# Performance work log

Hardware: AMD Instinct MI355X
Metric: run time of the kernel (lower is better)

The kernel has to match this reference:

```python
import jax, jax.numpy as jnp
import numpy as np

B, S, D = 8, 1024, 128
EPS = 1e-7
LN_EPS = 1e-3  # keras LayerNormalization default


def setup_inputs() -> dict:
    key = jax.random.key(0)
    ks = jax.random.split(key, 8)
    sd = 1.0 / np.sqrt(D)
    return {
        "x": jax.random.normal(ks[0], (B, S, D), jnp.float32),
        "Wq": jax.random.normal(ks[1], (D, D), jnp.float32) * sd,
        "bq": jnp.zeros((D,), jnp.float32),
        "Wm": jax.random.normal(ks[2], (D, D), jnp.float32) * sd,
        "bm": jnp.zeros((D,), jnp.float32),
        "Ww": jax.random.normal(ks[3], (D, 1), jnp.float32) * sd,
        "bw": jnp.zeros((1,), jnp.float32),
        "Wc": jax.random.normal(ks[4], (D, 1), jnp.float32) * sd,
        "bc": jnp.zeros((1,), jnp.float32),
        "emb_map": jax.random.normal(ks[5], (D, D, D), jnp.float32) * 0.02,
        "gamma": jnp.ones((D,), jnp.float32),
        "beta": jnp.zeros((D,), jnp.float32),
    }


def reference(x, Wq, bq, Wm, bm, Ww, bw, Wc, bc, emb_map, gamma, beta):
    b_, s_, d_ = x.shape
    q = x @ Wq + bq                      # [B,S,D]
    m = jax.nn.sigmoid(x @ Wm + bm)      # [B,S,D]
    w = jax.nn.relu(x @ Ww + bw)         # [B,S,1]
    c = jax.nn.relu(x @ Wc + bc)         # [B,S,1]

    # distances: for query pos i, preceding pos j (j<i) has distance i-j
    idx = jnp.arange(s_)
    dist = (idx[:, None] - idx[None, :]).astype(x.dtype)   # [S,S]
    valid = dist > 0                                       # strict causal
    # cosh positional decay, zero outside causal window -> [B,S,S]
    pe = jnp.where(valid[None], 1.0 / jnp.cosh((dist[None] - c) / (w + EPS)), 0.0)

    # angle between (pe * x_j * m_i + eps) and (q_i + eps), expanded analytically
    qp = q + EPS
    t1 = jnp.einsum('bjd,bid->bij', x, m * qp)             # sum_d x_j m_i q'_i
    s1 = jnp.einsum('bjd,bid->bij', x, m)                  # sum_d x_j m_i
    s2 = jnp.einsum('bjd,bid->bij', x * x, m * m)          # sum_d (x_j m_i)^2
    dot = pe * t1 + EPS * jnp.sum(qp, axis=-1)[:, :, None]
    na = jnp.sqrt(pe * pe * s2 + 2.0 * EPS * pe * s1 + d_ * EPS * EPS)
    nb = jnp.linalg.norm(qp, axis=-1)[:, :, None]
    cos = jnp.where(valid[None], dot / (na * nb), 0.0)
    angle = jnp.where(valid[None], jnp.arccos(cos), 0.0)   # [B,S,S]

    # query_result_i = sum_j pe*angle * x_j  -> [B,S,D]
    qr = jnp.einsum('bij,bjd->bid', pe * angle, x)

    # embedding matrix: current_token (rows) outer query_result (cols),
    # contracted against rank-3 map: out[b,s,d] = sum_{j,k} x[b,s,j] qr[b,s,k] map[d,j,k]
    em = jnp.einsum('bsj,bsk->bsjk', x, qr).reshape(b_, s_, d_ * d_)
    mapped = em @ emb_map.reshape(d_, d_ * d_).T           # [B,S,D]

    res = mapped + x
    mu = jnp.mean(res, axis=-1, keepdims=True)
    var = jnp.var(res, axis=-1, keepdims=True)
    out = (res - mu) / jnp.sqrt(var + LN_EPS) * gamma + beta
    return out  # dropout is identity at inference
```

## Files before the change

### kernel.cpp

```cpp
#include <hip/hip_runtime.h>
#include <hip/hip_bf16.h>
#include <math.h>

#define DD 128
#define SS 1024
#define NROWS 8192
#define EPSF 1e-7f
#define LN_EPSF 1e-3f
#define TCUT 30.0f

typedef __attribute__((ext_vector_type(8))) short bf16x8;
typedef __attribute__((ext_vector_type(8))) _Float16 f16x8;
typedef __attribute__((ext_vector_type(4))) float f32x4;
typedef __attribute__((ext_vector_type(16))) float f32x16;

__device__ __forceinline__ void gload_lds16(const void* g, void* l) {
    __builtin_amdgcn_global_load_lds(
        (const __attribute__((address_space(1))) unsigned int*)g,
        (__attribute__((address_space(3))) unsigned int*)l, 16, 0, 0);
}
__device__ __forceinline__ short f2bf(float v) {
    union { __hip_bfloat16 h; short s; } u;
    u.h = __float2bfloat16(v);
    return u.s;
}
__device__ __forceinline__ float bf2f(short s) {
    union { __hip_bfloat16 h; short s; } u; u.s = s;
    return __bfloat162float(u.h);
}
__device__ __forceinline__ short f2h(float v) {
    union { _Float16 h; short s; } u;
    u.h = (_Float16)v;
    return u.s;
}
__device__ __forceinline__ unsigned int pkmul_f16(unsigned int a, unsigned int b) {
    unsigned int r;
    asm("v_pk_mul_f16 %0, %1, %2" : "=v"(r) : "v"(a), "v"(b));
    return r;
}
__device__ __forceinline__ unsigned int f2h_dup(float v) {
    union { _Float16 h[2]; unsigned int u; } c;
    c.h[0] = (_Float16)v; c.h[1] = c.h[0];
    return c.u;
}

__global__ __launch_bounds__(256) void k0a_emb(const float* __restrict__ emb,
                                               short* __restrict__ embB) {
    __shared__ float lt[128][132];
    int j = blockIdx.x, t = threadIdx.x;
    {
        int d = t >> 1, kh = (t & 1) * 64;
        const float* src = emb + (size_t)d * 16384 + (size_t)j * 128 + kh;
#pragma unroll
        for (int q = 0; q < 16; ++q)
            *(float4*)&lt[d][kh + q * 4] = *(const float4*)(src + q * 4);
    }
    __syncthreads();
#pragma unroll
    for (int i = 0; i < 8; ++i) {
        int idx = i * 256 + t;
        int l = idx & 63, s = (idx >> 6) & 7, dt = (idx >> 9) & 3;
        const float* p = &lt[dt * 32 + (l & 31)][s * 16 + (l >> 5) * 8];
        union { bf16x8 v; short sa[8]; } ob;
#pragma unroll
        for (int e = 0; e < 8; ++e) ob.sa[e] = f2h(p[e]);
        *(bf16x8*)(embB + (size_t)j * 16384 + dt * 4096 + s * 512 + (size_t)l * 8) = ob.v;
    }
}

__global__ __launch_bounds__(256) void k0w_split(const float* __restrict__ Wq,
        const float* __restrict__ Wm, short* __restrict__ Wfrag) {
    int T = blockIdx.x * 256 + threadIdx.x;
    int e = T & 7, l = (T >> 3) & 63, ks = (T >> 9) & 3, nt = (T >> 11) & 7,
        mat = (T >> 14) & 1;
    int k = ks * 32 + ((l >> 4) & 3) * 8 + e;
    int c = nt * 16 + (l & 15);
    float v = (mat ? Wm : Wq)[k * 128 + c];
    short h = f2bf(v);
    float lo = v - bf2f(h);
    Wfrag[((((size_t)(mat * 2 + 0) * 8 + nt) * 4 + ks) * 64 + l) * 8 + e] = h;
    Wfrag[((((size_t)(mat * 2 + 1) * 8 + nt) * 4 + ks) * 64 + l) * 8 + e] = f2bf(lo);
}

__global__ __launch_bounds__(256) void k0c_xsplit(const float* __restrict__ x,
        const float* __restrict__ Ww, const float* __restrict__ bw,
        const float* __restrict__ Wc, const float* __restrict__ bc,
        short* __restrict__ xh2, short* __restrict__ xl2,
        float* __restrict__ scal) {
    __shared__ float xs[32][129];
    int rb = blockIdx.x, t = threadIdx.x;
    {
        int r = t >> 3, d0 = (t & 7) * 16;
        const float4* src = (const float4*)(x + (size_t)(rb * 32 + r) * 128 + d0);
#pragma unroll
        for (int q = 0; q < 4; ++q) *(float4*)&xs[r][d0 + q * 4] = src[q];
    }
    __syncthreads();
    int ks = (t >> 5) & 3, rf = t >> 7, l0 = (t & 31) * 2;
    union { bf16x8 v[2]; short s[16]; } hb, lb;
#pragma unroll
    for (int li = 0; li < 2; ++li) {
        int l = l0 + li;
        const float* p = &xs[rf * 16 + (l & 15)][ks * 32 + ((l >> 4) & 3) * 8];
#pragma unroll
        for (int e = 0; e < 8; ++e) {
            float v = p[e];
            short h = f2bf(v);
            hb.s[li * 8 + e] = h;
            lb.s[li * 8 + e] = f2bf(v - bf2f(h));
        }
    }
    {
        short* d1 = xh2 + (size_t)rb * 4096 + (size_t)t * 16;
        short* d2 = xl2 + (size_t)rb * 4096 + (size_t)t * 16;
        *(bf16x8*)d1 = hb.v[0]; *(bf16x8*)(d1 + 8) = hb.v[1];
        *(bf16x8*)d2 = lb.v[0]; *(bf16x8*)(d2 + 8) = lb.v[1];
    }
    int rr = t >> 3, seg = t & 7;
    float pw = 0.f, pc = 0.f;
#pragma unroll
    for (int dq = 0; dq < 16; ++dq) {
        float xv = xs[rr][seg * 16 + dq];
        pw = fmaf(xv, Ww[seg * 16 + dq], pw);
        pc = fmaf(xv, Wc[seg * 16 + dq], pc);
    }
    pw += __shfl_xor(pw, 1); pw += __shfl_xor(pw, 2); pw += __shfl_xor(pw, 4);
    pc += __shfl_xor(pc, 1); pc += __shfl_xor(pc, 2); pc += __shfl_xor(pc, 4);
    if (seg == 0) {
        scal[(size_t)(rb * 32 + rr) * 4 + 0] = fmaxf(pw + bw[0], 0.f);
        scal[(size_t)(rb * 32 + rr) * 4 + 1] = fmaxf(pc + bc[0], 0.f);
    }
}

__global__ __launch_bounds__(256) void k1_mfma(
    const short* __restrict__ xh2, const short* __restrict__ xl2,
    const short* __restrict__ Wfrag,
    const float* __restrict__ bq, const float* __restrict__ bm,
    float* __restrict__ mq, float* __restrict__ mo, float* __restrict__ scal)
{
    __shared__ __align__(16) short wl[65536];
    __shared__ float red[32][4][2];
    int t = threadIdx.x, w = t >> 6, l = t & 63;
    int l15 = l & 15, g = l >> 4;
    int row0 = blockIdx.x * 32;
#pragma unroll
    for (int it = 0; it < 32; ++it)
        gload_lds16(Wfrag + (size_t)(it * 256 + t) * 8, wl + (size_t)(it * 256 + w * 64) * 8);
    const short* xb  = xh2 + (size_t)blockIdx.x * 4096;
    const short* xlb = xl2 + (size_t)blockIdx.x * 4096;
    bf16x8 Ah[2][4], Al[2][4];
#pragma unroll
    for (int rf = 0; rf < 2; ++rf)
#pragma unroll
        for (int ks = 0; ks < 4; ++ks) {
            size_t o = ((size_t)(rf * 4 + ks) * 64 + l) * 8;
            Ah[rf][ks] = *(const bf16x8*)(xb + o);
            Al[rf][ks] = *(const bf16x8*)(xlb + o);
        }
    __syncthreads();
    f32x4 accq[2][2] = {}, accm[2][2] = {};
#pragma unroll
    for (int ntp = 0; ntp < 2; ++ntp) {
        int nt = w * 2 + ntp;
#pragma unroll
        for (int ks = 0; ks < 4; ++ks) {
            bf16x8 bhq = *(const bf16x8*)(wl + ((size_t)(0  + nt) * 4 + ks) * 512 + l * 8);
            bf16x8 blq = *(const bf16x8*)(wl + ((size_t)(8  + nt) * 4 + ks) * 512 + l * 8);
            bf16x8 bhm = *(const bf16x8*)(wl + ((size_t)(16 + nt) * 4 + ks) * 512 + l * 8);
            bf16x8 blm = *(const bf16x8*)(wl + ((size_t)(24 + nt) * 4 + ks) * 512 + l * 8);
#pragma unroll
            for (int rf = 0; rf < 2; ++rf) {
                accq[rf][ntp] = __builtin_amdgcn_mfma_f32_16x16x32_bf16(Ah[rf][ks], bhq, accq[rf][ntp], 0, 0, 0);
                accq[rf][ntp] = __builtin_amdgcn_mfma_f32_16x16x32_bf16(Ah[rf][ks], blq, accq[rf][ntp], 0, 0, 0);
                accq[rf][ntp] = __builtin_amdgcn_mfma_f32_16x16x32_bf16(Al[rf][ks], bhq, accq[rf][ntp], 0, 0, 0);
                accm[rf][ntp] = __builtin_amdgcn_mfma_f32_16x16x32_bf16(Ah[rf][ks], bhm, accm[rf][ntp], 0, 0, 0);
                accm[rf][ntp] = __builtin_amdgcn_mfma_f32_16x16x32_bf16(Ah[rf][ks], blm, accm[rf][ntp], 0, 0, 0);
                accm[rf][ntp] = __builtin_amdgcn_mfma_f32_16x16x32_bf16(Al[rf][ks], bhm, accm[rf][ntp], 0, 0, 0);
            }
        }
    }
    float sq1[2][4] = {{0,0,0,0},{0,0,0,0}};
    float sq2[2][4] = {{0,0,0,0},{0,0,0,0}};
#pragma unroll
    for (int ntp = 0; ntp < 2; ++ntp) {
        int c = (w * 2 + ntp) * 16 + l15;
        float bqv = bq[c] + EPSF, bmv = bm[c];
#pragma unroll
        for (int rf = 0; rf < 2; ++rf)
#pragma unroll
            for (int reg = 0; reg < 4; ++reg) {
                int rloc = rf * 16 + g * 4 + reg;
                float qp = accq[rf][ntp][reg] + bqv;
                float mv = 1.0f / (1.0f + expf(-(accm[rf][ntp][reg] + bmv)));
                size_t o = (size_t)(row0 + rloc) * 128 + c;
                mq[o] = mv * qp;
                mo[o] = mv;
                sq1[rf][reg] += qp;
                sq2[rf][reg] += qp * qp;
            }
    }
#pragma unroll
    for (int rf = 0; rf < 2; ++rf)
#pragma unroll
        for (int reg = 0; reg < 4; ++reg) {
            float a = sq1[rf][reg], b = sq2[rf][reg];
            a += __shfl_xor(a, 1); a += __shfl_xor(a, 2);
            a += __shfl_xor(a, 4); a += __shfl_xor(a, 8);
            b += __shfl_xor(b, 1); b += __shfl_xor(b, 2);
            b += __shfl_xor(b, 4); b += __shfl_xor(b, 8);
            if (l15 == 0) {
                red[rf * 16 + g * 4 + reg][w][0] = a;
                red[rf * 16 + g * 4 + reg][w][1] = b;
            }
        }
    __syncthreads();
    if (t < 32) {
        float a = red[t][0][0] + red[t][1][0] + red[t][2][0] + red[t][3][0];
        float b = red[t][0][1] + red[t][1][1] + red[t][2][1] + red[t][3][1];
        scal[(size_t)(row0 + t) * 4 + 2] = a;
        scal[(size_t)(row0 + t) * 4 + 3] = sqrtf(b);
    }
}

__global__ __launch_bounds__(256) void k2_qr(
    const float* __restrict__ x,
    const float* __restrict__ mq, const float* __restrict__ mo,
    const float* __restrict__ scal, short* __restrict__ qrh2)
{
    int row = blockIdx.x;
    int i = row & (SS - 1);
    const float* xb = x + (size_t)(row - i) * DD;
    int t = threadIdx.x, w = t >> 6, l = t & 63;
    int sub = l >> 4, q = l & 15;
    int qo = q * 8;

    float mqv[8], mov[8];
    {
        const float* mp = mq + (size_t)row * DD + qo;
        float4 a = *(const float4*)mp, b = *(const float4*)(mp + 4);
        mqv[0] = a.x; mqv[1] = a.y; mqv[2] = a.z; mqv[3] = a.w;
        mqv[4] = b.x; mqv[5] = b.y; mqv[6] = b.z; mqv[7] = b.w;
        const float* op = mo + (size_t)row * DD + qo;
        float4 c = *(const float4*)op, d = *(const float4*)(op + 4);
        mov[0] = c.x; mov[1] = c.y; mov[2] = c.z; mov[3] = c.w;
        mov[4] = d.x; mov[5] = d.y; mov[6] = d.z; mov[7] = d.w;
    }
    float wv = scal[row * 4 + 0], cv = scal[row * 4 + 1];
    float sumqp = scal[row * 4 + 2], nb = scal[row * 4 + 3];
    float wi = wv + EPSF;
    float dmaxf = cv + TCUT * wi;
    int dmax = (dmaxf >= (float)i) ? i : (int)dmaxf;

    float acc[8] = {0.f, 0.f, 0.f, 0.f, 0.f, 0.f, 0.f, 0.f};
    int nit = (dmax + 15) >> 4;
    int dbase = 1 + w * 4 + sub;
    for (int it = 0; it < nit; ++it) {
        int dist = dbase + it * 16;
        float xv[8];
        if (dist <= dmax) {
            const float* xp = xb + (size_t)(i - dist) * DD + qo;
            float4 a = *(const float4*)xp, b = *(const float4*)(xp + 4);
            xv[0] = a.x; xv[1] = a.y; xv[2] = a.z; xv[3] = a.w;
            xv[4] = b.x; xv[5] = b.y; xv[6] = b.z; xv[7] = b.w;
        } else {
#pragma unroll
            for (int e = 0; e < 8; ++e) xv[e] = 0.f;
        }
        float t1 = 0.f, s1 = 0.f, s2 = 0.f;
#pragma unroll
        for (int e = 0; e < 8; ++e) {
            float xm = xv[e] * mov[e];
            t1 = fmaf(xv[e], mqv[e], t1);
            s1 += xm;
            s2 = fmaf(xm, xm, s2);
        }
#pragma unroll
        for (int off = 1; off < 16; off <<= 1) {
            t1 += __shfl_xor(t1, off);
            s1 += __shfl_xor(s1, off);
            s2 += __shfl_xor(s2, off);
        }
        float tt = ((float)dist - cv) / wi;
        float pe = 1.0f / coshf(tt);
        float dotv = fmaf(pe, t1, EPSF * sumqp);
        float na = sqrtf(fmaf(pe * pe, s2,
                         fmaf(2.0f * EPSF * pe, s1, (float)DD * EPSF * EPSF)));
        float cosv = fminf(1.0f, fmaxf(-1.0f, dotv / (na * nb)));
        float ang = acosf(cosv);
        float wgt = pe * ang;
#pragma unroll
        for (int e = 0; e < 8; ++e) acc[e] = fmaf(wgt, xv[e], acc[e]);
    }
#pragma unroll
    for (int e = 0; e < 8; ++e) {
        acc[e] += __shfl_xor(acc[e], 16);
        acc[e] += __shfl_xor(acc[e], 32);
    }
    __shared__ float sq[4][DD];
    if (l < 16) {
#pragma unroll
        for (int e = 0; e < 8; ++e) sq[w][qo + e] = acc[e];
    }
    __syncthreads();
    if (t < DD) {
        float v = sq[0][t] + sq[1][t] + sq[2][t] + sq[3][t];
        int rbq = row >> 7, rr = row & 127, rt2 = rr >> 5, lp = rr & 31;
        int k = t;
        qrh2[(((size_t)(rbq * 4 + rt2) * 8 + (k >> 4)) * 64
              + (lp + 32 * ((k >> 3) & 1))) * 8 + (k & 7)] = f2h(v);
    }
}

__global__ __launch_bounds__(256, 2) void k3_gemm(
    const float* __restrict__ x, const short* __restrict__ embB,
    const short* __restrict__ qrh2, float* __restrict__ part)
{
    __shared__ unsigned int xtd[32][66];
    __shared__ float sof[64][128];
    int t = threadIdx.x, w = t >> 6, l = t & 63;
    int l31 = l & 31, hi = l >> 5;
    int dh = w & 1, sh = w >> 1;
    int rb = blockIdx.x, js = blockIdx.y;

    {
        int r = t >> 2, q = t & 3;
        const float* xp = x + (size_t)(rb * 64 + r) * 128 + js * 32 + q * 8;
        float4 a = *(const float4*)xp, b = *(const float4*)(xp + 4);
        xtd[q * 8 + 0][r] = f2h_dup(a.x); xtd[q * 8 + 1][r] = f2h_dup(a.y);
        xtd[q * 8 + 2][r] = f2h_dup(a.z); xtd[q * 8 + 3][r] = f2h_dup(a.w);
        xtd[q * 8 + 4][r] = f2h_dup(b.x); xtd[q * 8 + 5][r] = f2h_dup(b.y);
        xtd[q * 8 + 6][r] = f2h_dup(b.z); xtd[q * 8 + 7][r] = f2h_dup(b.w);
    }

    unsigned int qrp[2][4][4];
#pragma unroll
    for (int rt = 0; rt < 2; ++rt) {
        int R32 = rb * 2 + rt;
#pragma unroll
        for (int s = 0; s < 4; ++s) {
            union { f16x8 v; unsigned int u[4]; } qb;
            qb.v = *(const f16x8*)(qrh2
                + (((size_t)R32 * 8 + sh * 4 + s) * 64 + l) * 8);
#pragma unroll
            for (int p = 0; p < 4; ++p) qrp[rt][s][p] = qb.u[p];
        }
    }

    const short* Bbase = embB + (size_t)(js * 32) * 16384
                         + (size_t)(dh * 2) * 4096 + (size_t)(sh * 4) * 512
                         + (size_t)l * 8;

    f32x16 acc[2][2];
#pragma unroll
    for (int rt = 0; rt < 2; ++rt)
#pragma unroll
        for (int i = 0; i < 2; ++i)
#pragma unroll
            for (int q = 0; q < 16; ++q) acc[rt][i][q] = 0.f;

#define LOADB(BN, JJ)                                                       \
    {                                                                       \
        const short* bp_ = Bbase + (size_t)(JJ) * 16384;                    \
        _Pragma("unroll")                                                   \
        for (int i = 0; i < 2; ++i)                                         \
            _Pragma("unroll")                                               \
            for (int s = 0; s < 4; ++s)                                     \
                BN[i][s] = *(const f16x8*)(bp_ + i * 4096 + s * 512);       \
    }

#define COMPUTE(BN, JJ)                                                     \
    {                                                                       \
        unsigned int xs0 = xtd[JJ][l31], xs1 = xtd[JJ][32 + l31];           \
        _Pragma("unroll")                                                   \
        for (int s = 0; s < 4; ++s) {                                       \
            union { f16x8 v; unsigned int u[4]; } a0, a1;                   \
            _Pragma("unroll")                                               \
            for (int p = 0; p < 4; ++p) {                                   \
                a0.u[p] = pkmul_f16(qrp[0][s][p], xs0);                     \
                a1.u[p] = pkmul_f16(qrp[1][s][p], xs1);                     \
            }                                                               \
            acc[0][0] = __builtin_amdgcn_mfma_f32_32x32x16_f16(             \
                a0.v, BN[0][s], acc[0][0], 0, 0, 0);                        \
            acc[0][1] = __builtin_amdgcn_mfma_f32_32x32x16_f16(             \
                a0.v, BN[1][s], acc[0][1], 0, 0, 0);                        \
            acc[1][0] = __builtin_amdgcn_mfma_f32_32x32x16_f16(             \
                a1.v, BN[0][s], acc[1][0], 0, 0, 0);                        \
            acc[1][1] = __builtin_amdgcn_mfma_f32_32x32x16_f16(             \
                a1.v, BN[1][s], acc[1][1], 0, 0, 0);                        \
        }                                                                   \
    }

    f16x8 B0[2][4], B1[2][4];
    LOADB(B0, 0)
    __syncthreads();

#pragma unroll 1
    for (int jj = 0; jj < 32; jj += 2) {
        if (jj + 1 < 32) LOADB(B1, jj + 1)
        COMPUTE(B0, jj)
        if (jj + 2 < 32) LOADB(B0, jj + 2)
        COMPUTE(B1, jj + 1)
    }
#undef LOADB
#undef COMPUTE

    __syncthreads();
    if (sh == 0) {
#pragma unroll
        for (int rt = 0; rt < 2; ++rt)
#pragma unroll
            for (int i = 0; i < 2; ++i)
#pragma unroll
                for (int q = 0; q < 16; ++q) {
                    int r = rt * 32 + (q & 3) + 8 * (q >> 2) + 4 * hi;
                    sof[r][(dh * 2 + i) * 32 + l31] = acc[rt][i][q];
                }
    }
    __syncthreads();
    if (sh == 1) {
#pragma unroll
        for (int rt = 0; rt < 2; ++rt)
#pragma unroll
            for (int i = 0; i < 2; ++i)
#pragma unroll
                for (int q = 0; q < 16; ++q) {
                    int r = rt * 32 + (q & 3) + 8 * (q >> 2) + 4 * hi;
                    sof[r][(dh * 2 + i) * 32 + l31] += acc[rt][i][q];
                }
    }
    __syncthreads();
#pragma unroll
    for (int i = 0; i < 8; ++i) {
        int idx = i * 256 + t;
        int r = idx >> 5, c4 = (idx & 31) * 4;
        float4 v = *(const float4*)&sof[r][c4];
        *(float4*)(part + (size_t)js * (NROWS * DD)
                   + (size_t)(rb * 64 + r) * 128 + c4) = v;
    }
}

__global__ __launch_bounds__(256) void k4_ln(
    const float* __restrict__ x, const float* __restrict__ part,
    const float* __restrict__ gamma, const float* __restrict__ beta,
    float* __restrict__ out)
{
    int wave = threadIdx.x >> 6, lane = threadIdx.x & 63;
    int row = blockIdx.x * 4 + wave;
    size_t base = (size_t)row * DD;
    float r0 = x[base + lane], r1 = x[base + lane + 64];
#pragma unroll
    for (int p = 0; p < 4; ++p) {
        r0 += part[(size_t)p * NROWS * DD + base + lane];
        r1 += part[(size_t)p * NROWS * DD + base + lane + 64];
    }
    float s = r0 + r1, s2 = r0 * r0 + r1 * r1;
#pragma unroll
    for (int off = 32; off > 0; off >>= 1) {
        s += __shfl_xor(s, off);
        s2 += __shfl_xor(s2, off);
    }
    float mu = s * (1.0f / DD);
    float var = s2 * (1.0f / DD) - mu * mu;
    var = fmaxf(var, 0.0f);
    float rs = rsqrtf(var + LN_EPSF);
    out[base + lane] = (r0 - mu) * rs * gamma[lane] + beta[lane];
    out[base + lane + 64] = (r1 - mu) * rs * gamma[lane + 64] + beta[lane + 64];
}

extern "C" void kernel_launch(void* const* d_in, const int* in_sizes, int n_in,
                              void* d_out, int out_size, void* d_ws, size_t ws_size,
                              hipStream_t stream) {
    const float* x     = (const float*)d_in[0];
    const float* Wq    = (const float*)d_in[1];
    const float* bq    = (const float*)d_in[2];
    const float* Wm    = (const float*)d_in[3];
    const float* bm    = (const float*)d_in[4];
    const float* Ww    = (const float*)d_in[5];
    const float* bw    = (const float*)d_in[6];
    const float* Wc    = (const float*)d_in[7];
    const float* bc    = (const float*)d_in[8];
    const float* emb   = (const float*)d_in[9];
    const float* gamma = (const float*)d_in[10];
    const float* beta  = (const float*)d_in[11];
    float* out = (float*)d_out;
    float* ws  = (float*)d_ws;

    short* embB  = (short*)ws;
    short* qrh2  = (short*)(ws + 1048576);
    float* scal  = ws + 1572864;
    float* part  = ws + 1605632;
    float* tr    = ws + 1605632;
    short* xh2   = (short*)tr;
    short* xl2   = (short*)(tr + 524288);
    float* mq    = tr + 1048576;
    float* mo    = tr + 2097152;
    short* Wfrag = (short*)(tr + 3145728);

    hipLaunchKernelGGL(k0a_emb,   dim3(128),    dim3(256), 0, stream, emb, embB);
    hipLaunchKernelGGL(k0w_split, dim3(256),    dim3(256), 0, stream, Wq, Wm, Wfrag);
    hipLaunchKernelGGL(k0c_xsplit,dim3(256),    dim3(256), 0, stream,
                       x, Ww, bw, Wc, bc, xh2, xl2, scal);
    hipLaunchKernelGGL(k1_mfma,   dim3(256),    dim3(256), 0, stream,
                       xh2, xl2, Wfrag, bq, bm, mq, mo, scal);
    hipLaunchKernelGGL(k2_qr,     dim3(8192),   dim3(256), 0, stream,
                       x, mq, mo, scal, qrh2);
    hipLaunchKernelGGL(k3_gemm,   dim3(128, 4), dim3(256), 0, stream,
                       x, embB, qrh2, part);
    hipLaunchKernelGGL(k4_ln,     dim3(2048),   dim3(256), 0, stream,
                       x, part, gamma, beta, out);
}
```

Baseline: 90.84 us.

## Retile embedding GEMM with LDS double-buffered B and bf16 partial sums

```diff
diff --git a/kernel.cpp b/kernel.cpp
--- a/kernel.cpp
+++ b/kernel.cpp
@@ -42,6 +42,11 @@
     union { _Float16 h[2]; unsigned int u; } c;
     c.h[0] = (_Float16)v; c.h[1] = c.h[0];
     return c.u;
+}
+__device__ __forceinline__ unsigned int pack_bf16(float lo, float hi) {
+    unsigned int r;
+    asm("v_cvt_pk_bf16_f32 %0, %1, %2" : "=v"(r) : "v"(lo), "v"(hi));
+    return r;
 }
 
 __global__ __launch_bounds__(256) void k0a_emb(const float* __restrict__ emb,
@@ -313,43 +318,46 @@
 
 __global__ __launch_bounds__(256, 2) void k3_gemm(
     const float* __restrict__ x, const short* __restrict__ embB,
-    const short* __restrict__ qrh2, float* __restrict__ part)
+    const short* __restrict__ qrh2, short* __restrict__ partb)
 {
-    __shared__ unsigned int xtd[32][66];
-    __shared__ float sof[64][128];
+    __shared__ __align__(16) short bB[2][16384];
+    __shared__ unsigned int xtd[16][132];
     int t = threadIdx.x, w = t >> 6, l = t & 63;
     int l31 = l & 31, hi = l >> 5;
-    int dh = w & 1, sh = w >> 1;
+    int rh = w >> 1, dh = w & 1;
     int rb = blockIdx.x, js = blockIdx.y;
 
     {
-        int r = t >> 2, q = t & 3;
-        const float* xp = x + (size_t)(rb * 64 + r) * 128 + js * 32 + q * 8;
+        int r = t >> 1, jq = (t & 1) * 8;
+        const float* xp = x + (size_t)(rb * 128 + r) * 128 + js * 16 + jq;
         float4 a = *(const float4*)xp, b = *(const float4*)(xp + 4);
-        xtd[q * 8 + 0][r] = f2h_dup(a.x); xtd[q * 8 + 1][r] = f2h_dup(a.y);
-        xtd[q * 8 + 2][r] = f2h_dup(a.z); xtd[q * 8 + 3][r] = f2h_dup(a.w);
-        xtd[q * 8 + 4][r] = f2h_dup(b.x); xtd[q * 8 + 5][r] = f2h_dup(b.y);
-        xtd[q * 8 + 6][r] = f2h_dup(b.z); xtd[q * 8 + 7][r] = f2h_dup(b.w);
-    }
-
-    unsigned int qrp[2][4][4];
+        xtd[jq + 0][r] = f2h_dup(a.x); xtd[jq + 1][r] = f2h_dup(a.y);
+        xtd[jq + 2][r] = f2h_dup(a.z); xtd[jq + 3][r] = f2h_dup(a.w);
+        xtd[jq + 4][r] = f2h_dup(b.x); xtd[jq + 5][r] = f2h_dup(b.y);
+        xtd[jq + 6][r] = f2h_dup(b.z); xtd[jq + 7][r] = f2h_dup(b.w);
+    }
+
+    {
+        const short* src = embB + (size_t)(js * 16) * 16384;
+#pragma unroll
+        for (int i = 0; i < 8; ++i)
+            gload_lds16(src + (size_t)(i * 256 + t) * 8,
+                        &bB[0][0] + (size_t)(i * 256 + w * 64) * 8);
+    }
+
+    unsigned int qrp[2][8][4];
 #pragma unroll
     for (int rt = 0; rt < 2; ++rt) {
-        int R32 = rb * 2 + rt;
-#pragma unroll
-        for (int s = 0; s < 4; ++s) {
+        int R32 = rb * 4 + rh * 2 + rt;
+#pragma unroll
+        for (int s = 0; s < 8; ++s) {
             union { f16x8 v; unsigned int u[4]; } qb;
-            qb.v = *(const f16x8*)(qrh2
-                + (((size_t)R32 * 8 + sh * 4 + s) * 64 + l) * 8);
+            qb.v = *(const f16x8*)(qrh2 + (((size_t)R32 * 8 + s) * 64 + l) * 8);
 #pragma unroll
             for (int p = 0; p < 4; ++p) qrp[rt][s][p] = qb.u[p];
         }
     }
 
-    const short* Bbase = embB + (size_t)(js * 32) * 16384
-                         + (size_t)(dh * 2) * 4096 + (size_t)(sh * 4) * 512
-                         + (size_t)l * 8;
-
     f32x16 acc[2][2];
 #pragma unroll
     for (int rt = 0; rt < 2; ++rt)
@@ -358,89 +366,63 @@
 #pragma unroll
             for (int q = 0; q < 16; ++q) acc[rt][i][q] = 0.f;
 
-#define LOADB(BN, JJ)                                                       \
-    {                                                                       \
-        const short* bp_ = Bbase + (size_t)(JJ) * 16384;                    \
-        _Pragma("unroll")                                                   \
-        for (int i = 0; i < 2; ++i)                                         \
-            _Pragma("unroll")                                               \
-            for (int s = 0; s < 4; ++s)                                     \
-                BN[i][s] = *(const f16x8*)(bp_ + i * 4096 + s * 512);       \
-    }
-
-#define COMPUTE(BN, JJ)                                                     \
-    {                                                                       \
-        unsigned int xs0 = xtd[JJ][l31], xs1 = xtd[JJ][32 + l31];           \
-        _Pragma("unroll")                                                   \
-        for (int s = 0; s < 4; ++s) {                                       \
-            union { f16x8 v; unsigned int u[4]; } a0, a1;                   \
-            _Pragma("unroll")                                               \
-            for (int p = 0; p < 4; ++p) {                                   \
-                a0.u[p] = pkmul_f16(qrp[0][s][p], xs0);                     \
-                a1.u[p] = pkmul_f16(qrp[1][s][p], xs1);                     \
-            }                                                               \
-            acc[0][0] = __builtin_amdgcn_mfma_f32_32x32x16_f16(             \
-                a0.v, BN[0][s], acc[0][0], 0, 0, 0);                        \
-            acc[0][1] = __builtin_amdgcn_mfma_f32_32x32x16_f16(             \
-                a0.v, BN[1][s], acc[0][1], 0, 0, 0);                        \
-            acc[1][0] = __builtin_amdgcn_mfma_f32_32x32x16_f16(             \
-                a1.v, BN[0][s], acc[1][0], 0, 0, 0);                        \
-            acc[1][1] = __builtin_amdgcn_mfma_f32_32x32x16_f16(             \
-                a1.v, BN[1][s], acc[1][1], 0, 0, 0);                        \
-        }                                                                   \
-    }
-
-    f16x8 B0[2][4], B1[2][4];
-    LOADB(B0, 0)
     __syncthreads();
 
 #pragma unroll 1
-    for (int jj = 0; jj < 32; jj += 2) {
-        if (jj + 1 < 32) LOADB(B1, jj + 1)
-        COMPUTE(B0, jj)
-        if (jj + 2 < 32) LOADB(B0, jj + 2)
-        COMPUTE(B1, jj + 1)
-    }
-#undef LOADB
-#undef COMPUTE
-
-    __syncthreads();
-    if (sh == 0) {
-#pragma unroll
-        for (int rt = 0; rt < 2; ++rt)
-#pragma unroll
-            for (int i = 0; i < 2; ++i)
-#pragma unroll
-                for (int q = 0; q < 16; ++q) {
-                    int r = rt * 32 + (q & 3) + 8 * (q >> 2) + 4 * hi;
-                    sof[r][(dh * 2 + i) * 32 + l31] = acc[rt][i][q];
-                }
-    }
-    __syncthreads();
-    if (sh == 1) {
-#pragma unroll
-        for (int rt = 0; rt < 2; ++rt)
-#pragma unroll
-            for (int i = 0; i < 2; ++i)
-#pragma unroll
-                for (int q = 0; q < 16; ++q) {
-                    int r = rt * 32 + (q & 3) + 8 * (q >> 2) + 4 * hi;
-                    sof[r][(dh * 2 + i) * 32 + l31] += acc[rt][i][q];
-                }
-    }
-    __syncthreads();
+    for (int jj = 0; jj < 16; ++jj) {
+        int cur = jj & 1;
+        if (jj < 15) {
+            const short* src = embB + (size_t)(js * 16 + jj + 1) * 16384;
+#pragma unroll
+            for (int i = 0; i < 8; ++i)
+                gload_lds16(src + (size_t)(i * 256 + t) * 8,
+                            &bB[cur ^ 1][0] + (size_t)(i * 256 + w * 64) * 8);
+        }
+        unsigned int xs0 = xtd[jj][rh * 64 + l31];
+        unsigned int xs1 = xtd[jj][rh * 64 + 32 + l31];
+        const short* bb = &bB[cur][0] + (size_t)(dh * 2) * 4096 + (size_t)l * 8;
+#pragma unroll
+        for (int s = 0; s < 8; ++s) {
+            f16x8 Bd0 = *(const f16x8*)(bb + s * 512);
+            f16x8 Bd1 = *(const f16x8*)(bb + 4096 + s * 512);
+            union { f16x8 v; unsigned int u[4]; } a0, a1;
+#pragma unroll
+            for (int p = 0; p < 4; ++p) {
+                a0.u[p] = pkmul_f16(qrp[0][s][p], xs0);
+                a1.u[p] = pkmul_f16(qrp[1][s][p], xs1);
+            }
+            acc[0][0] = __builtin_amdgcn_mfma_f32_32x32x16_f16(a0.v, Bd0, acc[0][0], 0, 0, 0);
+            acc[0][1] = __builtin_amdgcn_mfma_f32_32x32x16_f16(a0.v, Bd1, acc[0][1], 0, 0, 0);
+            acc[1][0] = __builtin_amdgcn_mfma_f32_32x32x16_f16(a1.v, Bd0, acc[1][0], 0, 0, 0);
+            acc[1][1] = __builtin_amdgcn_mfma_f32_32x32x16_f16(a1.v, Bd1, acc[1][1], 0, 0, 0);
+        }
+        __syncthreads();
+    }
+
+    short* sofh = &bB[0][0];
+#pragma unroll
+    for (int rt = 0; rt < 2; ++rt)
+#pragma unroll
+        for (int i = 0; i < 2; ++i)
+#pragma unroll
+            for (int q = 0; q < 16; ++q) {
+                int r = rh * 64 + rt * 32 + (q & 3) + 8 * (q >> 2) + 4 * hi;
+                int c = dh * 64 + i * 32 + l31;
+                sofh[r * 136 + c] = f2h(0.f), sofh[r * 136 + c] = f2bf(acc[rt][i][q]);
+            }
+    __syncthreads();
+    size_t pbase = (size_t)js * ((size_t)NROWS * DD);
 #pragma unroll
     for (int i = 0; i < 8; ++i) {
         int idx = i * 256 + t;
-        int r = idx >> 5, c4 = (idx & 31) * 4;
-        float4 v = *(const float4*)&sof[r][c4];
-        *(float4*)(part + (size_t)js * (NROWS * DD)
-                   + (size_t)(rb * 64 + r) * 128 + c4) = v;
+        int r = idx >> 4, c8 = (idx & 15) * 8;
+        *(bf16x8*)(partb + pbase + (size_t)(rb * 128 + r) * 128 + c8)
+            = *(const bf16x8*)(sofh + r * 136 + c8);
     }
 }
 
 __global__ __launch_bounds__(256) void k4_ln(
-    const float* __restrict__ x, const float* __restrict__ part,
+    const float* __restrict__ x, const short* __restrict__ partb,
     const float* __restrict__ gamma, const float* __restrict__ beta,
     float* __restrict__ out)
 {
@@ -449,9 +431,9 @@
     size_t base = (size_t)row * DD;
     float r0 = x[base + lane], r1 = x[base + lane + 64];
 #pragma unroll
-    for (int p = 0; p < 4; ++p) {
-        r0 += part[(size_t)p * NROWS * DD + base + lane];
-        r1 += part[(size_t)p * NROWS * DD + base + lane + 64];
+    for (int p = 0; p < 8; ++p) {
+        r0 += bf2f(partb[(size_t)p * 1048576 + base + lane]);
+        r1 += bf2f(partb[(size_t)p * 1048576 + base + lane + 64]);
     }
     float s = r0 + r1, s2 = r0 * r0 + r1 * r1;
 #pragma unroll
@@ -488,7 +470,7 @@
     short* embB  = (short*)ws;
     short* qrh2  = (short*)(ws + 1048576);
     float* scal  = ws + 1572864;
-    float* part  = ws + 1605632;
+    short* partb = (short*)(ws + 1605632);
     float* tr    = ws + 1605632;
     short* xh2   = (short*)tr;
     short* xl2   = (short*)(tr + 524288);
@@ -504,8 +486,8 @@
                        xh2, xl2, Wfrag, bq, bm, mq, mo, scal);
     hipLaunchKernelGGL(k2_qr,     dim3(8192),   dim3(256), 0, stream,
                        x, mq, mo, scal, qrh2);
-    hipLaunchKernelGGL(k3_gemm,   dim3(128, 4), dim3(256), 0, stream,
-                       x, embB, qrh2, part);
+    hipLaunchKernelGGL(k3_gemm,   dim3(64, 8),  dim3(256), 0, stream,
+                       x, embB, qrh2, partb);
     hipLaunchKernelGGL(k4_ln,     dim3(2048),   dim3(256), 0, stream,
-                       x, part, gamma, beta, out);
-}
+                       x, partb, gamma, beta, out);
+}
```

New measurement: 87.98 us. 1.03x faster.
